# Kernel optimization log

Measured on AMD Instinct MI355X. Metric: run time of the kernel, lower is better.

## Reference

```python
import jax, jax.numpy as jnp
import numpy as np

N = 50000        # num nodes
E = 800000       # num edges (avg degree 16)
NFEAT = 128
NHID = 128
NCLASS = 64


def setup_inputs() -> dict:
    key = jax.random.key(0)
    k0, k1, k2, k3 = jax.random.split(key, 4)
    x = jax.random.normal(k0, (N, NFEAT), dtype=jnp.float32)
    edge_index = jax.random.randint(k1, (2, E), 0, N)
    edge_weight = jnp.ones((E,), dtype=jnp.float32)
    # GCNConv linear weights (glorot-ish uniform), biases zero
    s1 = 1.0 / np.sqrt(NFEAT)
    W1 = jax.random.uniform(k2, (NFEAT, NHID), jnp.float32, -s1, s1)
    b1 = jnp.zeros((NHID,), jnp.float32)
    s2 = 1.0 / np.sqrt(NHID)
    W2 = jax.random.uniform(k3, (NHID, NCLASS), jnp.float32, -s2, s2)
    b2 = jnp.zeros((NCLASS,), jnp.float32)
    return {"x": x, "edge_index": edge_index, "edge_weight": edge_weight,
            "W1": W1, "b1": b1, "W2": W2, "b2": b2}


def reference(x, edge_index, edge_weight, W1, b1, W2, b2):
    n = x.shape[0]
    # add self loops (fill_value = 1.0), as GCNConv(add_self_loops=True)
    loops = jnp.arange(n)
    ei = jnp.concatenate([edge_index, jnp.stack([loops, loops])], axis=1)
    ew = jnp.concatenate([edge_weight, jnp.ones((n,), x.dtype)])
    row, col = ei[0], ei[1]
    # symmetric gcn normalization: D^-1/2 A D^-1/2
    deg = jax.ops.segment_sum(ew, col, num_segments=n)
    dinv = jnp.where(deg > 0, jax.lax.rsqrt(deg), 0.0)
    norm = dinv[row] * ew * dinv[col]        # [E+N]

    def conv(h, W, b):
        h = h @ W                                   # [N, F_out]
        msg = norm[:, None] * h[row]                # gather + scale, [E+N, F_out]
        return jax.ops.segment_sum(msg, col, num_segments=n) + b

    h = jax.nn.relu(conv(x, W1, b1))  # dropout p=0.0 -> identity
    out = conv(h, W2, b2)
    # F.normalize(p=2, dim=-1)
    nrm = jnp.linalg.norm(out, axis=-1, keepdims=True)
    return out / jnp.maximum(nrm, 1e-12)
```

## Files before the change

kernel.cpp:

```cpp
#include <hip/hip_runtime.h>

#define NF 128
#define NC 64
#define SLICES 64

typedef short bf16x8 __attribute__((ext_vector_type(8)));
typedef float f32x4 __attribute__((ext_vector_type(4)));

__device__ __forceinline__ unsigned f2bf(float f) {
    unsigned u = __float_as_uint(f);
    return (u + 0x7FFFu + ((u >> 16) & 1u)) >> 16;
}
__device__ __forceinline__ float bf2f(unsigned h) { return __uint_as_float(h << 16); }

__global__ __launch_bounds__(256) void prep_fused(const int* __restrict__ col,
                                                  unsigned short* __restrict__ eoff16,
                                                  unsigned short* __restrict__ C16,
                                                  const float* __restrict__ W1,
                                                  const float* __restrict__ W2,
                                                  unsigned short* __restrict__ Wt1,
                                                  unsigned short* __restrict__ Wt2,
                                                  const float* __restrict__ X,
                                                  unsigned* __restrict__ Xb2,
                                                  int N, int E, int SL, int nh,
                                                  int CRB, int WTB, int XCB) {
    __shared__ unsigned hist[12544];
    const int b = blockIdx.x;
    const int tid = threadIdx.x;
    if (b < CRB) {
        const int j = b >> 1;
        const int h = b & 1;
        const int nlo = h * nh;
        const int nhi = min(N, nlo + nh);
        const int words = (nhi - nlo + 1) >> 1;
        for (int i = tid; i < words; i += 256) hist[i] = 0;
        __syncthreads();
        const int e0 = j * SL, e1 = min(E, e0 + SL);
        for (int e = e0 + tid; e < e1; e += 256) {
            int c = col[e];
            if (c >= nlo && c < nhi) {
                int cl = c - nlo;
                unsigned sh = (cl & 1) * 16;
                unsigned old = atomicAdd(&hist[cl >> 1], 1u << sh);
                eoff16[e] = (unsigned short)((old >> sh) & 0xffffu);
            }
        }
        __syncthreads();
        unsigned* Cw = (unsigned*)(C16 + (size_t)j * N + nlo);
        for (int i = tid; i < words; i += 256) Cw[i] = hist[i];
    } else if (b < CRB + WTB) {
        int i = (b - CRB) * 256 + tid;
        if (i < 128 * 128) {
            int k = i >> 7, n = i & 127;
            Wt1[n * 128 + k] = (unsigned short)f2bf(W1[i]);
        } else {
            int j = i - 128 * 128;
            if (j < 128 * 64) {
                int k = j >> 6, n = j & 63;
                Wt2[n * 128 + k] = (unsigned short)f2bf(W2[j]);
            }
        }
    } else {
        const float4* X4 = (const float4*)X;
        uint2* O = (uint2*)Xb2;
        int items = N * 32;
        for (int i = (b - CRB - WTB) * 256 + tid; i < items; i += XCB * 256) {
            float4 v = X4[i];
            O[i] = make_uint2(f2bf(v.x) | (f2bf(v.y) << 16),
                              f2bf(v.z) | (f2bf(v.w) << 16));
        }
    }
}

__global__ __launch_bounds__(256) void scanC_kernel(unsigned short* __restrict__ C16,
                                                    int* __restrict__ tot, int N) {
    int n = blockIdx.x * 256 + threadIdx.x;
    if (n >= N) return;
    int t = 0;
#pragma unroll 4
    for (int j = 0; j < SLICES; ++j) {
        size_t idx = (size_t)j * N + n;
        int v = C16[idx];
        C16[idx] = (unsigned short)t;
        t += v;
    }
    tot[n] = t;
}

__global__ __launch_bounds__(256) void scan_blocks(const int* __restrict__ cnt,
                                                   int* __restrict__ excl,
                                                   int* __restrict__ bsum, int N) {
    __shared__ int sh[256];
    int t = threadIdx.x;
    int base = blockIdx.x * 1024 + t * 4;
    int v0 = base + 0 < N ? cnt[base + 0] : 0;
    int v1 = base + 1 < N ? cnt[base + 1] : 0;
    int v2 = base + 2 < N ? cnt[base + 2] : 0;
    int v3 = base + 3 < N ? cnt[base + 3] : 0;
    int s = v0 + v1 + v2 + v3;
    sh[t] = s;
    __syncthreads();
    for (int off = 1; off < 256; off <<= 1) {
        int x = (t >= off) ? sh[t - off] : 0;
        __syncthreads();
        sh[t] += x;
        __syncthreads();
    }
    int incl = sh[t];
    int exclT = incl - s;
    if (t == 255) bsum[blockIdx.x] = incl;
    if (base + 0 < N) excl[base + 0] = exclT;
    if (base + 1 < N) excl[base + 1] = exclT + v0;
    if (base + 2 < N) excl[base + 2] = exclT + v0 + v1;
    if (base + 3 < N) excl[base + 3] = exclT + v0 + v1 + v2;
}

__global__ void scan_sums(int* __restrict__ bsum, int nb) {
    int run = 0;
    for (int i = 0; i < nb; ++i) { int v = bsum[i]; bsum[i] = run; run += v; }
    bsum[nb] = run;
}

__global__ __launch_bounds__(256) void scan_add(int* __restrict__ excl,
                                                const int* __restrict__ bsum,
                                                int N, int nb) {
    int i = blockIdx.x * 256 + threadIdx.x;
    if (i < N) excl[i] += bsum[i >> 10];
    if (i == 0) excl[N] = bsum[nb];
}

__global__ __launch_bounds__(256) void scatter_gemm1_fused(const int* __restrict__ row,
                                                           const int* __restrict__ col,
                                                           const float* __restrict__ ew,
                                                           const int* __restrict__ rowPtr,
                                                           const unsigned short* __restrict__ Coff16,
                                                           const unsigned short* __restrict__ eoff16,
                                                           unsigned* __restrict__ csru,
                                                           const unsigned short* __restrict__ Xb,
                                                           const unsigned short* __restrict__ Wt1,
                                                           unsigned short* __restrict__ H,
                                                           int N, int E, int SL, int SB) {
    __shared__ char XsB[16384];
    __shared__ char WsB[32768];
    const int tid = threadIdx.x;
    if ((int)blockIdx.x < SB) {
        const int j = blockIdx.x >> 3;
        const int sub = blockIdx.x & 7;
        const int e0 = j * SL, e1 = min(E, e0 + SL);
        const int per = ((e1 - e0) + 7) >> 3;
        const int lo = min(e1, e0 + sub * per);
        const int hi = min(e1, lo + per);
        const unsigned short* Crow = Coff16 + (size_t)j * N;
        for (int e = lo + tid; e < hi; e += 256) {
            int c = col[e];
            int idx = rowPtr[c] + (int)Crow[c] + (int)eoff16[e];
            csru[idx] = ((unsigned)row[e] << 16) | f2bf(ew[e]);
        }
        return;
    }
    const int bm0 = ((int)blockIdx.x - SB) * 64;
    {
        int r = tid >> 2, q4 = (tid & 3) * 4;
        const uint4* src = (const uint4*)(Xb + (size_t)min(bm0 + r, N - 1) * 128);
#pragma unroll
        for (int qq = 0; qq < 4; ++qq) {
            int kb = (q4 + qq) * 16;
            *(uint4*)(XsB + r * 256 + (kb ^ ((r & 7) << 4))) = src[q4 + qq];
        }
    }
    {
        const uint4* src = (const uint4*)Wt1;
#pragma unroll
        for (int t = 0; t < 8; ++t) {
            int i = t * 256 + tid;
            int n = i >> 4, kb = (i & 15) * 16;
            *(uint4*)(WsB + n * 256 + (kb ^ ((n & 7) << 4))) = src[i];
        }
    }
    __syncthreads();
    const int w = tid >> 6, l = tid & 63;
    const int lr = l & 15, lg = l >> 4;
    f32x4 acc[8] = {};
#pragma unroll
    for (int kk = 0; kk < 4; ++kk) {
        int r = w * 16 + lr;
        bf16x8 a = *(const bf16x8*)(XsB + r * 256 + ((kk * 64 + lg * 16) ^ ((r & 7) << 4)));
        bf16x8 b[8];
#pragma unroll
        for (int nt = 0; nt < 8; ++nt) {
            int n = nt * 16 + lr;
            b[nt] = *(const bf16x8*)(WsB + n * 256 + ((kk * 64 + lg * 16) ^ ((n & 7) << 4)));
        }
#pragma unroll
        for (int nt = 0; nt < 8; ++nt)
            acc[nt] = __builtin_amdgcn_mfma_f32_16x16x32_bf16(a, b[nt], acc[nt], 0, 0, 0);
    }
#pragma unroll
    for (int reg = 0; reg < 4; ++reg) {
        int node = bm0 + w * 16 + lg * 4 + reg;
        if (node < N) {
#pragma unroll
            for (int nt = 0; nt < 8; ++nt)
                H[(size_t)node * 128 + nt * 16 + lr] = (unsigned short)f2bf(acc[nt][reg]);
        }
    }
}

__global__ __launch_bounds__(256) void gemm2_mfma(const unsigned short* __restrict__ A,
                                                  const unsigned short* __restrict__ Wt2,
                                                  unsigned short* __restrict__ H, int N) {
    __shared__ char XsB[32768];
    __shared__ char WsB[16384];
    const int tid = threadIdx.x;
    const int bm0 = blockIdx.x * 128;
    {
        int k16 = tid & 15, r0 = tid >> 4;
        for (int it = 0; it < 8; ++it) {
            int r = it * 16 + r0;
            int node = min(bm0 + r, N - 1);
            uint4 g = *(const uint4*)(A + (size_t)node * 128 + k16 * 8);
            *(uint4*)(XsB + r * 256 + ((k16 * 16) ^ ((r & 7) << 4))) = g;
        }
    }
    {
        const uint4* src = (const uint4*)Wt2;
        for (int t = 0; t < 4; ++t) {
            int i = t * 256 + tid;
            int n = i >> 4, kb = (i & 15) * 16;
            *(uint4*)(WsB + n * 256 + (kb ^ ((n & 7) << 4))) = src[i];
        }
    }
    __syncthreads();
    const int w = tid >> 6, l = tid & 63;
    const int lr = l & 15, lg = l >> 4;
    f32x4 acc[2][4] = {};
#pragma unroll
    for (int kk = 0; kk < 4; ++kk) {
        bf16x8 a[2], b[4];
#pragma unroll
        for (int mt = 0; mt < 2; ++mt) {
            int r = w * 32 + mt * 16 + lr;
            a[mt] = *(const bf16x8*)(XsB + r * 256 + ((kk * 64 + lg * 16) ^ ((r & 7) << 4)));
        }
#pragma unroll
        for (int nt = 0; nt < 4; ++nt) {
            int n = nt * 16 + lr;
            b[nt] = *(const bf16x8*)(WsB + n * 256 + ((kk * 64 + lg * 16) ^ ((n & 7) << 4)));
        }
#pragma unroll
        for (int mt = 0; mt < 2; ++mt)
#pragma unroll
            for (int nt = 0; nt < 4; ++nt)
                acc[mt][nt] = __builtin_amdgcn_mfma_f32_16x16x32_bf16(a[mt], b[nt], acc[mt][nt], 0, 0, 0);
    }
#pragma unroll
    for (int mt = 0; mt < 2; ++mt)
#pragma unroll
        for (int reg = 0; reg < 4; ++reg) {
            int node = bm0 + w * 32 + mt * 16 + lg * 4 + reg;
            if (node < N) {
#pragma unroll
                for (int nt = 0; nt < 4; ++nt)
                    H[(size_t)node * 64 + nt * 16 + lr] = (unsigned short)f2bf(acc[mt][nt][reg]);
            }
        }
}

__global__ __launch_bounds__(256) void deg_dinv_kernel(const int* __restrict__ rowPtr,
                                                       const unsigned* __restrict__ csru,
                                                       float* __restrict__ dinv, int N) {
    int idx = blockIdx.x * 256 + threadIdx.x;
    int n = idx >> 4, l = idx & 15;
    if (n >= N) return;
    int beg = rowPtr[n], end = rowPtr[n + 1];
    float s = 0.f;
    for (int i = beg + l; i < end; i += 16) s += bf2f(csru[i] & 0xffffu);
#pragma unroll
    for (int off = 8; off; off >>= 1) s += __shfl_xor(s, off, 16);
    if (l == 0) dinv[n] = rsqrtf(s + 1.0f);
}

__global__ __launch_bounds__(256) void agg_gather1(const int* __restrict__ rowPtr,
                                                   const unsigned* __restrict__ csru,
                                                   const unsigned* __restrict__ H1u,
                                                   const float* __restrict__ dinv,
                                                   const float2* __restrict__ b2,
                                                   unsigned* __restrict__ out1, int N) {
    int n = (blockIdx.x * 256 + threadIdx.x) >> 6;
    int lane = threadIdx.x & 63;
    if (n >= N) return;
    float dn = dinv[n];
    float accx = 0.f, accy = 0.f;
    int beg = rowPtr[n], end = rowPtr[n + 1];
    int j = beg;
    for (; j + 4 <= end; j += 4) {
        unsigned p0 = csru[j + 0], p1 = csru[j + 1], p2 = csru[j + 2], p3 = csru[j + 3];
        int s0 = p0 >> 16, s1 = p1 >> 16, s2 = p2 >> 16, s3 = p3 >> 16;
        float w0 = bf2f(p0 & 0xffffu) * dinv[s0];
        float w1 = bf2f(p1 & 0xffffu) * dinv[s1];
        float w2 = bf2f(p2 & 0xffffu) * dinv[s2];
        float w3 = bf2f(p3 & 0xffffu) * dinv[s3];
        unsigned v0 = H1u[(size_t)s0 * 64 + lane];
        unsigned v1 = H1u[(size_t)s1 * 64 + lane];
        unsigned v2 = H1u[(size_t)s2 * 64 + lane];
        unsigned v3 = H1u[(size_t)s3 * 64 + lane];
        accx += w0 * bf2f(v0 & 0xffffu); accy += w0 * bf2f(v0 >> 16);
        accx += w1 * bf2f(v1 & 0xffffu); accy += w1 * bf2f(v1 >> 16);
        accx += w2 * bf2f(v2 & 0xffffu); accy += w2 * bf2f(v2 >> 16);
        accx += w3 * bf2f(v3 & 0xffffu); accy += w3 * bf2f(v3 >> 16);
    }
    for (; j < end; ++j) {
        unsigned p = csru[j];
        int s0 = p >> 16;
        float w = bf2f(p & 0xffffu) * dinv[s0];
        unsigned v = H1u[(size_t)s0 * 64 + lane];
        accx += w * bf2f(v & 0xffffu); accy += w * bf2f(v >> 16);
    }
    unsigned hv = H1u[(size_t)n * 64 + lane];
    float2 bb = b2[lane];
    float s = dn * dn;
    float ox = fmaxf(fmaf(dn, accx, s * bf2f(hv & 0xffffu)) + bb.x, 0.f);
    float oy = fmaxf(fmaf(dn, accy, s * bf2f(hv >> 16)) + bb.y, 0.f);
    out1[(size_t)n * 64 + lane] = f2bf(ox) | (f2bf(oy) << 16);
}

__global__ __launch_bounds__(256) void agg_gather2(const int* __restrict__ rowPtr,
                                                   const unsigned* __restrict__ csru,
                                                   const unsigned* __restrict__ H3u,
                                                   const float* __restrict__ dinv,
                                                   const float2* __restrict__ b2,
                                                   float2* __restrict__ out2, int N) {
    int n = (blockIdx.x * 256 + threadIdx.x) >> 5;
    int l = threadIdx.x & 31;
    if (n >= N) return;
    float dn = dinv[n];
    float accx = 0.f, accy = 0.f;
    int beg = rowPtr[n], end = rowPtr[n + 1];
    int j = beg;
    for (; j + 4 <= end; j += 4) {
        unsigned p0 = csru[j + 0], p1 = csru[j + 1], p2 = csru[j + 2], p3 = csru[j + 3];
        int s0 = p0 >> 16, s1 = p1 >> 16, s2 = p2 >> 16, s3 = p3 >> 16;
        float w0 = bf2f(p0 & 0xffffu) * dinv[s0];
        float w1 = bf2f(p1 & 0xffffu) * dinv[s1];
        float w2 = bf2f(p2 & 0xffffu) * dinv[s2];
        float w3 = bf2f(p3 & 0xffffu) * dinv[s3];
        unsigned v0 = H3u[(size_t)s0 * 32 + l];
        unsigned v1 = H3u[(size_t)s1 * 32 + l];
        unsigned v2 = H3u[(size_t)s2 * 32 + l];
        unsigned v3 = H3u[(size_t)s3 * 32 + l];
        accx += w0 * bf2f(v0 & 0xffffu); accy += w0 * bf2f(v0 >> 16);
        accx += w1 * bf2f(v1 & 0xffffu); accy += w1 * bf2f(v1 >> 16);
        accx += w2 * bf2f(v2 & 0xffffu); accy += w2 * bf2f(v2 >> 16);
        accx += w3 * bf2f(v3 & 0xffffu); accy += w3 * bf2f(v3 >> 16);
    }
    for (; j < end; ++j) {
        unsigned p = csru[j];
        int s0 = p >> 16;
        float w = bf2f(p & 0xffffu) * dinv[s0];
        unsigned v = H3u[(size_t)s0 * 32 + l];
        accx += w * bf2f(v & 0xffffu); accy += w * bf2f(v >> 16);
    }
    unsigned hv = H3u[(size_t)n * 32 + l];
    float2 bb = b2[l];
    float s = dn * dn;
    float vx = fmaf(dn, accx, s * bf2f(hv & 0xffffu)) + bb.x;
    float vy = fmaf(dn, accy, s * bf2f(hv >> 16)) + bb.y;
    float ss = vx * vx + vy * vy;
#pragma unroll
    for (int off = 16; off; off >>= 1) ss += __shfl_xor(ss, off, 64);
    float scale = 1.0f / fmaxf(sqrtf(ss), 1e-12f);
    out2[(size_t)n * 32 + l] = make_float2(vx * scale, vy * scale);
}

extern "C" void kernel_launch(void* const* d_in, const int* in_sizes, int n_in,
                              void* d_out, int out_size, void* d_ws, size_t ws_size,
                              hipStream_t stream) {
    const float* x  = (const float*)d_in[0];
    const int*   ei = (const int*)d_in[1];
    const float* ew = (const float*)d_in[2];
    const float* W1 = (const float*)d_in[3];
    const float* b1 = (const float*)d_in[4];
    const float* W2 = (const float*)d_in[5];
    const float* b2 = (const float*)d_in[6];
    float* out = (float*)d_out;
    const int N = in_sizes[0] / NF;
    const int E = in_sizes[2];
    const int* row = ei;
    const int* col = ei + E;
    const int NB = (N + 1023) / 1024;
    const int SL = (E + SLICES - 1) / SLICES;
    const int nh = (N + 1) / 2;

    char* ws = (char*)d_ws;
    size_t off = 0;
    auto take = [&](size_t bytes) {
        char* p = ws + off;
        off = (off + bytes + 255) & ~(size_t)255;
        return p;
    };
    float* dinv   = (float*)take((size_t)N * 4);
    int*   tot    = (int*)  take((size_t)N * 4);
    int*   rowPtr = (int*)  take((size_t)(N + 1) * 4);
    unsigned short* eoff16 = (unsigned short*)take((size_t)E * 2);
    int*   bsum   = (int*)  take((size_t)(NB + 1) * 4);
    unsigned short* C16    = (unsigned short*)take((size_t)SLICES * N * 2);
    unsigned* csru = (unsigned*)take((size_t)E * 4);
    unsigned short* Xb   = (unsigned short*)take((size_t)N * NF * 2);
    unsigned short* H1   = (unsigned short*)take((size_t)N * NF * 2);
    unsigned short* relu = (unsigned short*)take((size_t)N * NF * 2);
    unsigned short* Wt1  = (unsigned short*)take(128 * 128 * 2);
    unsigned short* Wt2  = (unsigned short*)take(64 * 128 * 2);
    unsigned short* H3 = H1;

    const int CRB = 2 * SLICES, WTB = 96, XCB = 1024;
    prep_fused<<<CRB + WTB + XCB, 256, 0, stream>>>(col, eoff16, C16, W1, W2, Wt1, Wt2,
                                                    x, (unsigned*)Xb, N, E, SL, nh,
                                                    CRB, WTB, XCB);

    scanC_kernel<<<(N + 255) / 256, 256, 0, stream>>>(C16, tot, N);
    scan_blocks<<<NB, 256, 0, stream>>>(tot, rowPtr, bsum, N);
    scan_sums<<<1, 1, 0, stream>>>(bsum, NB);
    scan_add<<<(N + 255) / 256, 256, 0, stream>>>(rowPtr, bsum, N, NB);

    const int SB = 8 * SLICES;
    const int GB = (N + 63) / 64;
    scatter_gemm1_fused<<<SB + GB, 256, 0, stream>>>(row, col, ew, rowPtr, C16, eoff16,
                                                     csru, Xb, Wt1, H1, N, E, SL, SB);

    deg_dinv_kernel<<<(N * 16 + 255) / 256, 256, 0, stream>>>(rowPtr, csru, dinv, N);

    agg_gather1<<<(N * 64 + 255) / 256, 256, 0, stream>>>(rowPtr, csru, (const unsigned*)H1,
                                                          dinv, (const float2*)b1,
                                                          (unsigned*)relu, N);

    gemm2_mfma<<<(N + 127) / 128, 256, 0, stream>>>(relu, Wt2, H3, N);
    agg_gather2<<<(N * 32 + 255) / 256, 256, 0, stream>>>(rowPtr, csru, (const unsigned*)H3,
                                                          dinv, (const float2*)b2,
                                                          (float2*)out, N);
}
```

Measured before the change: 149.4 us.

## Chunk H1 into column slabs and prescale edge weights by source dinv

GEMM1 now writes H1 as four column chunks of 32 features each, stored contiguously per node. The first aggregation uses 16 lanes per node and loops over the four chunks, so each gather pass touches a smaller working set that fits better in L2. A new kernel multiplies each CSR edge weight by dinv of its source once and stores it back as bf16, which removes the dependent dinv gathers from both aggregation kernels. In exchange, edge lists are re-read four times, there is one extra launch, and the extra bf16 rounding of the prescaled weights slightly reduces precision.

Result: slower. 165.7 us (+10.9%).

```diff
diff --git a/kernel.cpp b/kernel.cpp
--- a/kernel.cpp
+++ b/kernel.cpp
@@ -138,7 +138,7 @@
                                                            unsigned* __restrict__ csru,
                                                            const unsigned short* __restrict__ Xb,
                                                            const unsigned short* __restrict__ Wt1,
-                                                           unsigned short* __restrict__ H,
+                                                           unsigned short* __restrict__ H1c,
                                                            int N, int E, int SL, int SB) {
     __shared__ char XsB[16384];
     __shared__ char WsB[32768];
@@ -201,7 +201,8 @@
         if (node < N) {
 #pragma unroll
             for (int nt = 0; nt < 8; ++nt)
-                H[(size_t)node * 128 + nt * 16 + lr] = (unsigned short)f2bf(acc[nt][reg]);
+                H1c[((size_t)(nt >> 1) * N + node) * 32 + (nt & 1) * 16 + lr] =
+                    (unsigned short)f2bf(acc[nt][reg]);
         }
     }
 }
@@ -280,48 +281,57 @@
     if (l == 0) dinv[n] = rsqrtf(s + 1.0f);
 }
 
+__global__ __launch_bounds__(256) void norm_w_kernel(unsigned* __restrict__ csru,
+                                                     const float* __restrict__ dinv, int E) {
+    int i = blockIdx.x * 256 + threadIdx.x;
+    if (i >= E) return;
+    unsigned p = csru[i];
+    float w = bf2f(p & 0xffffu) * dinv[p >> 16];
+    csru[i] = (p & 0xffff0000u) | f2bf(w);
+}
+
 __global__ __launch_bounds__(256) void agg_gather1(const int* __restrict__ rowPtr,
                                                    const unsigned* __restrict__ csru,
-                                                   const unsigned* __restrict__ H1u,
+                                                   const unsigned* __restrict__ H1c,
                                                    const float* __restrict__ dinv,
                                                    const float2* __restrict__ b2,
                                                    unsigned* __restrict__ out1, int N) {
-    int n = (blockIdx.x * 256 + threadIdx.x) >> 6;
-    int lane = threadIdx.x & 63;
+    int n = blockIdx.x * 16 + (threadIdx.x >> 4);
+    int l = threadIdx.x & 15;
     if (n >= N) return;
     float dn = dinv[n];
-    float accx = 0.f, accy = 0.f;
+    float s = dn * dn;
     int beg = rowPtr[n], end = rowPtr[n + 1];
-    int j = beg;
-    for (; j + 4 <= end; j += 4) {
-        unsigned p0 = csru[j + 0], p1 = csru[j + 1], p2 = csru[j + 2], p3 = csru[j + 3];
-        int s0 = p0 >> 16, s1 = p1 >> 16, s2 = p2 >> 16, s3 = p3 >> 16;
-        float w0 = bf2f(p0 & 0xffffu) * dinv[s0];
-        float w1 = bf2f(p1 & 0xffffu) * dinv[s1];
-        float w2 = bf2f(p2 & 0xffffu) * dinv[s2];
-        float w3 = bf2f(p3 & 0xffffu) * dinv[s3];
-        unsigned v0 = H1u[(size_t)s0 * 64 + lane];
-        unsigned v1 = H1u[(size_t)s1 * 64 + lane];
-        unsigned v2 = H1u[(size_t)s2 * 64 + lane];
-        unsigned v3 = H1u[(size_t)s3 * 64 + lane];
-        accx += w0 * bf2f(v0 & 0xffffu); accy += w0 * bf2f(v0 >> 16);
-        accx += w1 * bf2f(v1 & 0xffffu); accy += w1 * bf2f(v1 >> 16);
-        accx += w2 * bf2f(v2 & 0xffffu); accy += w2 * bf2f(v2 >> 16);
-        accx += w3 * bf2f(v3 & 0xffffu); accy += w3 * bf2f(v3 >> 16);
-    }
-    for (; j < end; ++j) {
-        unsigned p = csru[j];
-        int s0 = p >> 16;
-        float w = bf2f(p & 0xffffu) * dinv[s0];
-        unsigned v = H1u[(size_t)s0 * 64 + lane];
-        accx += w * bf2f(v & 0xffffu); accy += w * bf2f(v >> 16);
-    }
-    unsigned hv = H1u[(size_t)n * 64 + lane];
-    float2 bb = b2[lane];
-    float s = dn * dn;
-    float ox = fmaxf(fmaf(dn, accx, s * bf2f(hv & 0xffffu)) + bb.x, 0.f);
-    float oy = fmaxf(fmaf(dn, accy, s * bf2f(hv >> 16)) + bb.y, 0.f);
-    out1[(size_t)n * 64 + lane] = f2bf(ox) | (f2bf(oy) << 16);
+#pragma unroll
+    for (int c = 0; c < 4; ++c) {
+        const unsigned* P = H1c + (size_t)c * N * 16;
+        float accx = 0.f, accy = 0.f;
+        int j = beg;
+        for (; j + 4 <= end; j += 4) {
+            unsigned p0 = csru[j + 0], p1 = csru[j + 1], p2 = csru[j + 2], p3 = csru[j + 3];
+            float w0 = bf2f(p0 & 0xffffu), w1 = bf2f(p1 & 0xffffu);
+            float w2 = bf2f(p2 & 0xffffu), w3 = bf2f(p3 & 0xffffu);
+            unsigned v0 = P[(size_t)(p0 >> 16) * 16 + l];
+            unsigned v1 = P[(size_t)(p1 >> 16) * 16 + l];
+            unsigned v2 = P[(size_t)(p2 >> 16) * 16 + l];
+            unsigned v3 = P[(size_t)(p3 >> 16) * 16 + l];
+            accx += w0 * bf2f(v0 & 0xffffu); accy += w0 * bf2f(v0 >> 16);
+            accx += w1 * bf2f(v1 & 0xffffu); accy += w1 * bf2f(v1 >> 16);
+            accx += w2 * bf2f(v2 & 0xffffu); accy += w2 * bf2f(v2 >> 16);
+            accx += w3 * bf2f(v3 & 0xffffu); accy += w3 * bf2f(v3 >> 16);
+        }
+        for (; j < end; ++j) {
+            unsigned p = csru[j];
+            float w = bf2f(p & 0xffffu);
+            unsigned v = P[(size_t)(p >> 16) * 16 + l];
+            accx += w * bf2f(v & 0xffffu); accy += w * bf2f(v >> 16);
+        }
+        unsigned hv = P[(size_t)n * 16 + l];
+        float2 bb = b2[c * 16 + l];
+        float ox = fmaxf(fmaf(dn, accx, s * bf2f(hv & 0xffffu)) + bb.x, 0.f);
+        float oy = fmaxf(fmaf(dn, accy, s * bf2f(hv >> 16)) + bb.y, 0.f);
+        out1[(size_t)n * 64 + c * 16 + l] = f2bf(ox) | (f2bf(oy) << 16);
+    }
 }
 
 __global__ __launch_bounds__(256) void agg_gather2(const int* __restrict__ rowPtr,
@@ -339,15 +349,12 @@
     int j = beg;
     for (; j + 4 <= end; j += 4) {
         unsigned p0 = csru[j + 0], p1 = csru[j + 1], p2 = csru[j + 2], p3 = csru[j + 3];
-        int s0 = p0 >> 16, s1 = p1 >> 16, s2 = p2 >> 16, s3 = p3 >> 16;
-        float w0 = bf2f(p0 & 0xffffu) * dinv[s0];
-        float w1 = bf2f(p1 & 0xffffu) * dinv[s1];
-        float w2 = bf2f(p2 & 0xffffu) * dinv[s2];
-        float w3 = bf2f(p3 & 0xffffu) * dinv[s3];
-        unsigned v0 = H3u[(size_t)s0 * 32 + l];
-        unsigned v1 = H3u[(size_t)s1 * 32 + l];
-        unsigned v2 = H3u[(size_t)s2 * 32 + l];
-        unsigned v3 = H3u[(size_t)s3 * 32 + l];
+        float w0 = bf2f(p0 & 0xffffu), w1 = bf2f(p1 & 0xffffu);
+        float w2 = bf2f(p2 & 0xffffu), w3 = bf2f(p3 & 0xffffu);
+        unsigned v0 = H3u[(size_t)(p0 >> 16) * 32 + l];
+        unsigned v1 = H3u[(size_t)(p1 >> 16) * 32 + l];
+        unsigned v2 = H3u[(size_t)(p2 >> 16) * 32 + l];
+        unsigned v3 = H3u[(size_t)(p3 >> 16) * 32 + l];
         accx += w0 * bf2f(v0 & 0xffffu); accy += w0 * bf2f(v0 >> 16);
         accx += w1 * bf2f(v1 & 0xffffu); accy += w1 * bf2f(v1 >> 16);
         accx += w2 * bf2f(v2 & 0xffffu); accy += w2 * bf2f(v2 >> 16);
@@ -355,9 +362,8 @@
     }
     for (; j < end; ++j) {
         unsigned p = csru[j];
-        int s0 = p >> 16;
-        float w = bf2f(p & 0xffffu) * dinv[s0];
-        unsigned v = H3u[(size_t)s0 * 32 + l];
+        float w = bf2f(p & 0xffffu);
+        unsigned v = H3u[(size_t)(p >> 16) * 32 + l];
         accx += w * bf2f(v & 0xffffu); accy += w * bf2f(v >> 16);
     }
     unsigned hv = H3u[(size_t)n * 32 + l];
@@ -406,11 +412,11 @@
     unsigned short* C16    = (unsigned short*)take((size_t)SLICES * N * 2);
     unsigned* csru = (unsigned*)take((size_t)E * 4);
     unsigned short* Xb   = (unsigned short*)take((size_t)N * NF * 2);
-    unsigned short* H1   = (unsigned short*)take((size_t)N * NF * 2);
+    unsigned short* H1c  = (unsigned short*)take((size_t)N * NF * 2);
     unsigned short* relu = (unsigned short*)take((size_t)N * NF * 2);
     unsigned short* Wt1  = (unsigned short*)take(128 * 128 * 2);
     unsigned short* Wt2  = (unsigned short*)take(64 * 128 * 2);
-    unsigned short* H3 = H1;
+    unsigned short* H3 = H1c;
 
     const int CRB = 2 * SLICES, WTB = 96, XCB = 1024;
     prep_fused<<<CRB + WTB + XCB, 256, 0, stream>>>(col, eoff16, C16, W1, W2, Wt1, Wt2,
@@ -425,11 +431,12 @@
     const int SB = 8 * SLICES;
     const int GB = (N + 63) / 64;
     scatter_gemm1_fused<<<SB + GB, 256, 0, stream>>>(row, col, ew, rowPtr, C16, eoff16,
-                                                     csru, Xb, Wt1, H1, N, E, SL, SB);
+                                                     csru, Xb, Wt1, H1c, N, E, SL, SB);
 
     deg_dinv_kernel<<<(N * 16 + 255) / 256, 256, 0, stream>>>(rowPtr, csru, dinv, N);
-
-    agg_gather1<<<(N * 64 + 255) / 256, 256, 0, stream>>>(rowPtr, csru, (const unsigned*)H1,
+    norm_w_kernel<<<(E + 255) / 256, 256, 0, stream>>>(csru, dinv, E);
+
+    agg_gather1<<<(N * 16 + 255) / 256, 256, 0, stream>>>(rowPtr, csru, (const unsigned*)H1c,
                                                           dinv, (const float2*)b1,
                                                           (unsigned*)relu, N);
 
```

## Prefold source dinv into CSR edge weights and unroll gathers by eight

Applied to the files above, without the earlier changes.

Adds a pass that multiplies each packed CSR edge weight by dinv of its source node and stores it back as bf16. Both aggregation kernels can then skip the per-edge dinv gather. Their main loops are unrolled from 4 to 8 edges, with all indices loaded before the feature gathers to raise memory-level parallelism. In exchange this costs an extra kernel launch and a read-modify-write over all edges, rounds the combined weight to bf16, and uses more registers per thread.

Result: slower. 155.5 us (+4.1%).

```diff
diff --git a/kernel.cpp b/kernel.cpp
--- a/kernel.cpp
+++ b/kernel.cpp
@@ -280,6 +280,15 @@
     if (l == 0) dinv[n] = rsqrtf(s + 1.0f);
 }
 
+__global__ __launch_bounds__(256) void norm_w_kernel(unsigned* __restrict__ csru,
+                                                     const float* __restrict__ dinv, int E) {
+    int i = blockIdx.x * 256 + threadIdx.x;
+    if (i >= E) return;
+    unsigned p = csru[i];
+    float w = bf2f(p & 0xffffu) * dinv[p >> 16];
+    csru[i] = (p & 0xffff0000u) | f2bf(w);
+}
+
 __global__ __launch_bounds__(256) void agg_gather1(const int* __restrict__ rowPtr,
                                                    const unsigned* __restrict__ csru,
                                                    const unsigned* __restrict__ H1u,
@@ -293,27 +302,24 @@
     float accx = 0.f, accy = 0.f;
     int beg = rowPtr[n], end = rowPtr[n + 1];
     int j = beg;
-    for (; j + 4 <= end; j += 4) {
-        unsigned p0 = csru[j + 0], p1 = csru[j + 1], p2 = csru[j + 2], p3 = csru[j + 3];
-        int s0 = p0 >> 16, s1 = p1 >> 16, s2 = p2 >> 16, s3 = p3 >> 16;
-        float w0 = bf2f(p0 & 0xffffu) * dinv[s0];
-        float w1 = bf2f(p1 & 0xffffu) * dinv[s1];
-        float w2 = bf2f(p2 & 0xffffu) * dinv[s2];
-        float w3 = bf2f(p3 & 0xffffu) * dinv[s3];
-        unsigned v0 = H1u[(size_t)s0 * 64 + lane];
-        unsigned v1 = H1u[(size_t)s1 * 64 + lane];
-        unsigned v2 = H1u[(size_t)s2 * 64 + lane];
-        unsigned v3 = H1u[(size_t)s3 * 64 + lane];
-        accx += w0 * bf2f(v0 & 0xffffu); accy += w0 * bf2f(v0 >> 16);
-        accx += w1 * bf2f(v1 & 0xffffu); accy += w1 * bf2f(v1 >> 16);
-        accx += w2 * bf2f(v2 & 0xffffu); accy += w2 * bf2f(v2 >> 16);
-        accx += w3 * bf2f(v3 & 0xffffu); accy += w3 * bf2f(v3 >> 16);
+    for (; j + 8 <= end; j += 8) {
+        unsigned p[8];
+        unsigned v[8];
+#pragma unroll
+        for (int q = 0; q < 8; ++q) p[q] = csru[j + q];
+#pragma unroll
+        for (int q = 0; q < 8; ++q) v[q] = H1u[(size_t)(p[q] >> 16) * 64 + lane];
+#pragma unroll
+        for (int q = 0; q < 8; ++q) {
+            float w = bf2f(p[q] & 0xffffu);
+            accx += w * bf2f(v[q] & 0xffffu);
+            accy += w * bf2f(v[q] >> 16);
+        }
     }
     for (; j < end; ++j) {
         unsigned p = csru[j];
-        int s0 = p >> 16;
-        float w = bf2f(p & 0xffffu) * dinv[s0];
-        unsigned v = H1u[(size_t)s0 * 64 + lane];
+        float w = bf2f(p & 0xffffu);
+        unsigned v = H1u[(size_t)(p >> 16) * 64 + lane];
         accx += w * bf2f(v & 0xffffu); accy += w * bf2f(v >> 16);
     }
     unsigned hv = H1u[(size_t)n * 64 + lane];
@@ -337,27 +343,24 @@
     float accx = 0.f, accy = 0.f;
     int beg = rowPtr[n], end = rowPtr[n + 1];
     int j = beg;
-    for (; j + 4 <= end; j += 4) {
-        unsigned p0 = csru[j + 0], p1 = csru[j + 1], p2 = csru[j + 2], p3 = csru[j + 3];
-        int s0 = p0 >> 16, s1 = p1 >> 16, s2 = p2 >> 16, s3 = p3 >> 16;
-        float w0 = bf2f(p0 & 0xffffu) * dinv[s0];
-        float w1 = bf2f(p1 & 0xffffu) * dinv[s1];
-        float w2 = bf2f(p2 & 0xffffu) * dinv[s2];
-        float w3 = bf2f(p3 & 0xffffu) * dinv[s3];
-        unsigned v0 = H3u[(size_t)s0 * 32 + l];
-        unsigned v1 = H3u[(size_t)s1 * 32 + l];
-        unsigned v2 = H3u[(size_t)s2 * 32 + l];
-        unsigned v3 = H3u[(size_t)s3 * 32 + l];
-        accx += w0 * bf2f(v0 & 0xffffu); accy += w0 * bf2f(v0 >> 16);
-        accx += w1 * bf2f(v1 & 0xffffu); accy += w1 * bf2f(v1 >> 16);
-        accx += w2 * bf2f(v2 & 0xffffu); accy += w2 * bf2f(v2 >> 16);
-        accx += w3 * bf2f(v3 & 0xffffu); accy += w3 * bf2f(v3 >> 16);
+    for (; j + 8 <= end; j += 8) {
+        unsigned p[8];
+        unsigned v[8];
+#pragma unroll
+        for (int q = 0; q < 8; ++q) p[q] = csru[j + q];
+#pragma unroll
+        for (int q = 0; q < 8; ++q) v[q] = H3u[(size_t)(p[q] >> 16) * 32 + l];
+#pragma unroll
+        for (int q = 0; q < 8; ++q) {
+            float w = bf2f(p[q] & 0xffffu);
+            accx += w * bf2f(v[q] & 0xffffu);
+            accy += w * bf2f(v[q] >> 16);
+        }
     }
     for (; j < end; ++j) {
         unsigned p = csru[j];
-        int s0 = p >> 16;
-        float w = bf2f(p & 0xffffu) * dinv[s0];
-        unsigned v = H3u[(size_t)s0 * 32 + l];
+        float w = bf2f(p & 0xffffu);
+        unsigned v = H3u[(size_t)(p >> 16) * 32 + l];
         accx += w * bf2f(v & 0xffffu); accy += w * bf2f(v >> 16);
     }
     unsigned hv = H3u[(size_t)n * 32 + l];
@@ -428,6 +431,7 @@
                                                      csru, Xb, Wt1, H1, N, E, SL, SB);
 
     deg_dinv_kernel<<<(N * 16 + 255) / 256, 256, 0, stream>>>(rowPtr, csru, dinv, N);
+    norm_w_kernel<<<(E + 255) / 256, 256, 0, stream>>>(csru, dinv, E);
 
     agg_gather1<<<(N * 64 + 255) / 256, 256, 0, stream>>>(rowPtr, csru, (const unsigned*)H1,
                                                           dinv, (const float2*)b1,
```
